# Performance work log

Measured on AMD Instinct MI355X. Metric: run time of the kernel, lower is better.

## Reference

```python
import jax, jax.numpy as jnp
import numpy as np

N_NODES = 100000
N_EDGES = 1600000
IN_C, HID_C, OUT_C = 128, 128, 64


def gcn_conv(x, W, b, src, dst, n_nodes):
    """PyG-style GCNConv: h = x @ W; add self-loops; symmetric deg^-1/2 norm;
    scatter-add aggregation; + bias. Self-loop contribution added analytically
    (norm for self-loop edge i->i is deg_i^-1) instead of materializing edges."""
    h = x @ W  # [N, C_out]
    # degree over dst including self-loops (edge weights are all ones)
    deg = jax.ops.segment_sum(jnp.ones((src.shape[0],), h.dtype), dst,
                              num_segments=n_nodes) + 1.0
    dinv = jax.lax.rsqrt(deg)  # deg >= 1 always
    norm = dinv[src] * dinv[dst]  # [E]
    agg = jax.ops.segment_sum(h[src] * norm[:, None], dst, num_segments=n_nodes)
    agg = agg + h * (dinv * dinv)[:, None]  # self-loop term
    return agg + b


def setup_inputs() -> dict:
    key = jax.random.key(0)
    k0, k1, k2, k3, k4, k5 = jax.random.split(key, 6)
    x = jax.random.normal(k0, (N_NODES, IN_C), dtype=jnp.float32)
    edge_index = jax.random.randint(k1, (2, N_EDGES), 0, N_NODES, dtype=jnp.int64)
    s1 = 1.0 / np.sqrt(IN_C)
    s2 = 1.0 / np.sqrt(HID_C)
    W1 = jax.random.uniform(k2, (IN_C, HID_C), jnp.float32, -s1, s1)
    b1 = jax.random.uniform(k3, (HID_C,), jnp.float32, -s1, s1)
    W2 = jax.random.uniform(k4, (HID_C, OUT_C), jnp.float32, -s2, s2)
    b2 = jax.random.uniform(k5, (OUT_C,), jnp.float32, -s2, s2)
    return {"x": x, "W1": W1, "b1": b1, "W2": W2, "b2": b2,
            "edge_index": edge_index}


def reference(x, W1, b1, W2, b2, edge_index):
    src, dst = edge_index[0], edge_index[1]
    h = gcn_conv(x, W1, b1, src, dst, N_NODES)
    h = jax.nn.relu(h)
    out = gcn_conv(h, W2, b2, src, dst, N_NODES)
    return out
```

## Files before the change

kernel.cpp:

```cpp
#include <hip/hip_runtime.h>


static constexpr int BSHIFT = 7;
static constexpr int BWIDTH = 1 << BSHIFT;
static constexpr int MAXBUCK = 2048;
static constexpr int NPART = 256;

static constexpr size_t OFF_ROW  = 458752;
static constexpr size_t OFF_CCNT = 925696;
static constexpr size_t OFF_COFF = 937984;
static constexpr size_t OFF_DINV = 962560;
static constexpr size_t OFF_CSR  = 1376256;
static constexpr size_t OFF_HS1  = 8388608;
static constexpr size_t OFF_OUT1 = 35651584;
static constexpr size_t OFF_HS2  = 62914560;
static constexpr size_t OFF_H2   = 75714560;
static constexpr size_t OFF_W1S  = 77811712;
static constexpr size_t OFF_W2S  = 77844480;

__device__ __forceinline__ unsigned short f2bf(float f) {
    unsigned u = __float_as_uint(f);
    u += 0x7fffu + ((u >> 16) & 1u);
    return (unsigned short)(u >> 16);
}

typedef __attribute__((ext_vector_type(8))) short bf16x8;
typedef __attribute__((ext_vector_type(4))) float f32x4;

__device__ __forceinline__ unsigned detect_flag(const unsigned* __restrict__ w) {
    unsigned fl = 0;
#pragma unroll
    for (int k = 1; k < 32; k += 2) fl |= w[k];
    return fl;
}

__device__ __forceinline__ int edge_dst(const unsigned* w, unsigned flag,
                                        int e, int E) {
    return flag ? (int)w[E + e] : (int)w[2 * E + 2 * e];
}
__device__ __forceinline__ int edge_src(const unsigned* w, unsigned flag,
                                        int e, int E) {
    return flag ? (int)w[e] : (int)w[2 * e];
}

__global__ __launch_bounds__(1024) void hist_wprep_kernel(
    const unsigned* __restrict__ w, unsigned* __restrict__ ccnt,
    unsigned* __restrict__ h2, int E, int nbuck,
    const float* __restrict__ W1, const float* __restrict__ W2,
    unsigned short* __restrict__ O1, unsigned short* __restrict__ O2) {
    if (blockIdx.x >= NPART) {
        const int which = blockIdx.x - NPART;
        const float* W = which ? W2 : W1;
        unsigned short* O = which ? O2 : O1;
        const int BN = which ? 64 : 128;
        const int total = 128 * BN / 4;
        for (int g = threadIdx.x; g < total; g += 1024) {
            int n = g % BN, k0 = (g / BN) * 4;
            ushort4 u;
            u.x = f2bf(W[(size_t)(k0 + 0) * BN + n]);
            u.y = f2bf(W[(size_t)(k0 + 1) * BN + n]);
            u.z = f2bf(W[(size_t)(k0 + 2) * BN + n]);
            u.w = f2bf(W[(size_t)(k0 + 3) * BN + n]);
            int off = ((((n >> 4) * 4 + (k0 >> 5)) * 16 + (n & 15)) * 4 +
                       ((k0 >> 3) & 3)) * 8 + (k0 & 4);
            *(ushort4*)(O + off) = u;
        }
        return;
    }
    __shared__ unsigned hist[MAXBUCK];
    for (int i = threadIdx.x; i < nbuck; i += 1024) hist[i] = 0;
    __syncthreads();
    const unsigned f = detect_flag(w);
    const int per = (E + NPART - 1) / NPART;
    const int e0 = blockIdx.x * per, e1 = min(E, e0 + per);
    for (int e = e0 + (int)threadIdx.x; e < e1; e += 1024)
        atomicAdd(&hist[edge_dst(w, f, e, E) >> BSHIFT], 1u);
    __syncthreads();
    for (int i = threadIdx.x; i < nbuck; i += 1024) {
        unsigned h = hist[i];
        h2[(size_t)i * NPART + blockIdx.x] = h;
        if (h) atomicAdd(&ccnt[i], h);
    }
}

__global__ __launch_bounds__(NPART) void scanoff_kernel(
    const unsigned* __restrict__ ccnt, unsigned* __restrict__ coff,
    unsigned* __restrict__ h2, int nbuck) {
    __shared__ unsigned red[NPART];
    __shared__ unsigned sh[NPART];
    const int b = blockIdx.x, t = threadIdx.x;
    unsigned p = 0;
    for (int i = t; i < b; i += NPART) p += ccnt[i];
    red[t] = p;
    __syncthreads();
#pragma unroll
    for (int off = NPART / 2; off > 0; off >>= 1) {
        if (t < off) red[t] += red[t + off];
        __syncthreads();
    }
    const unsigned coffb = red[0];
    if (t == 0) {
        coff[b] = coffb;
        if (b == nbuck - 1) coff[nbuck] = coffb + ccnt[b];
    }
    unsigned v = h2[(size_t)b * NPART + t];
    sh[t] = v;
    __syncthreads();
#pragma unroll
    for (int off = 1; off < NPART; off <<= 1) {
        unsigned a = (t >= off) ? sh[t - off] : 0u;
        __syncthreads();
        sh[t] += a;
        __syncthreads();
    }
    h2[(size_t)b * NPART + t] = coffb + sh[t] - v;
}

__global__ __launch_bounds__(1024) void partition_kernel(
    const unsigned* __restrict__ w, const unsigned* __restrict__ h2,
    unsigned* __restrict__ part, int E, int nbuck) {
    __shared__ unsigned lcur[MAXBUCK];
    for (int i = threadIdx.x; i < nbuck; i += 1024)
        lcur[i] = h2[(size_t)i * NPART + blockIdx.x];
    __syncthreads();
    const unsigned f = detect_flag(w);
    const int per = (E + NPART - 1) / NPART;
    const int e0 = blockIdx.x * per, e1 = min(E, e0 + per);
    for (int e = e0 + (int)threadIdx.x; e < e1; e += 1024) {
        int d = edge_dst(w, f, e, E);
        int s = edge_src(w, f, e, E);
        unsigned pos = atomicAdd(&lcur[d >> BSHIFT], 1u);
        part[pos] = (unsigned)s | ((unsigned)(d & (BWIDTH - 1)) << 20);
    }
}

template <int BN, bool ABF16, bool SCALE>
__device__ __forceinline__ void gemm_body(
    const void* __restrict__ Av, const unsigned short* __restrict__ Bs,
    const float* __restrict__ dinv, unsigned short* __restrict__ out,
    int M, int row0, int t) {
    constexpr int NT = BN / 16;
    const int w = t >> 6, lane = t & 63;
    const int m = lane & 15, q = lane >> 4;
    const int fb = (m * 4 + q) * 8;

    const int r0 = row0 + (2 * w) * 16 + m;
    const int r1 = r0 + 16;

    f32x4 acc[2][NT];
#pragma unroll
    for (int lt = 0; lt < 2; lt++)
#pragma unroll
        for (int nt = 0; nt < NT; nt++) acc[lt][nt] = (f32x4){0.f, 0.f, 0.f, 0.f};

#pragma unroll
    for (int ks = 0; ks < 4; ks++) {
        const int k0 = ks * 32 + q * 8;
        bf16x8 a0 = (bf16x8){0, 0, 0, 0, 0, 0, 0, 0};
        bf16x8 a1 = (bf16x8){0, 0, 0, 0, 0, 0, 0, 0};
        if (ABF16) {
            const unsigned short* A = (const unsigned short*)Av;
            if (r0 < M) a0 = *(const bf16x8*)(A + (size_t)r0 * 128 + k0);
            if (r1 < M) a1 = *(const bf16x8*)(A + (size_t)r1 * 128 + k0);
        } else {
            const float* A = (const float*)Av;
            if (r0 < M) {
                const float* p = A + (size_t)r0 * 128 + k0;
                f32x4 lo = *(const f32x4*)p, hi = *(const f32x4*)(p + 4);
                a0[0] = (short)f2bf(lo[0]); a0[1] = (short)f2bf(lo[1]);
                a0[2] = (short)f2bf(lo[2]); a0[3] = (short)f2bf(lo[3]);
                a0[4] = (short)f2bf(hi[0]); a0[5] = (short)f2bf(hi[1]);
                a0[6] = (short)f2bf(hi[2]); a0[7] = (short)f2bf(hi[3]);
            }
            if (r1 < M) {
                const float* p = A + (size_t)r1 * 128 + k0;
                f32x4 lo = *(const f32x4*)p, hi = *(const f32x4*)(p + 4);
                a1[0] = (short)f2bf(lo[0]); a1[1] = (short)f2bf(lo[1]);
                a1[2] = (short)f2bf(lo[2]); a1[3] = (short)f2bf(lo[3]);
                a1[4] = (short)f2bf(hi[0]); a1[5] = (short)f2bf(hi[1]);
                a1[6] = (short)f2bf(hi[2]); a1[7] = (short)f2bf(hi[3]);
            }
        }
#pragma unroll
        for (int nt = 0; nt < NT; nt++) {
            bf16x8 b = *(const bf16x8*)(Bs + (nt * 4 + ks) * 512 + fb);
            acc[0][nt] = __builtin_amdgcn_mfma_f32_16x16x32_bf16(a0, b, acc[0][nt], 0, 0, 0);
            acc[1][nt] = __builtin_amdgcn_mfma_f32_16x16x32_bf16(a1, b, acc[1][nt], 0, 0, 0);
        }
    }

#pragma unroll
    for (int lt = 0; lt < 2; lt++) {
#pragma unroll
        for (int r = 0; r < 4; r++) {
            int row = row0 + w * 32 + lt * 16 + q * 4 + r;
            if (row < M) {
                float s = SCALE ? dinv[row] : 1.0f;
#pragma unroll
                for (int nt = 0; nt < NT; nt++)
                    out[(size_t)row * BN + nt * 16 + m] = f2bf(acc[lt][nt][r] * s);
            }
        }
    }
}

template <int BN, bool ABF16>
__global__ __launch_bounds__(256) void gemm_mfma(
    const void* __restrict__ Av, const unsigned short* __restrict__ Bs,
    const float* __restrict__ dinv, unsigned short* __restrict__ out, int M) {
    gemm_body<BN, ABF16, true>(Av, Bs, dinv, out, M, blockIdx.x * 128,
                               threadIdx.x);
}

__global__ __launch_bounds__(256, 4) void bucket_gemm_kernel(
    const unsigned* __restrict__ part, const unsigned* __restrict__ coff,
    unsigned* __restrict__ row, float* __restrict__ dinv,
    int* __restrict__ csr, int N, int nbuck,
    const float* __restrict__ x, const unsigned short* __restrict__ w1s,
    unsigned short* __restrict__ hs1) {
    __shared__ unsigned cnt[BWIDTH];
    __shared__ unsigned sc[BWIDTH];
    __shared__ unsigned cur[BWIDTH];
    const int bid = blockIdx.x, t = threadIdx.x;
    if (bid >= nbuck) {
        gemm_body<128, false, false>(x, w1s, nullptr, hs1, N,
                                     (bid - nbuck) * 128, t);
        return;
    }
    const int b = bid, base = b << BSHIFT;
    if (t < BWIDTH) cnt[t] = 0;
    __syncthreads();
    const int e0 = (int)coff[b], e1 = (int)coff[b + 1];
    for (int e = e0 + t; e < e1; e += 256)
        atomicAdd(&cnt[part[e] >> 20], 1u);
    __syncthreads();
    if (t < BWIDTH) sc[t] = cnt[t];
    __syncthreads();
#pragma unroll
    for (int off = 1; off < BWIDTH; off <<= 1) {
        unsigned a = (t < BWIDTH && t >= off) ? sc[t - off] : 0u;
        __syncthreads();
        if (t < BWIDTH) sc[t] += a;
        __syncthreads();
    }
    if (t < BWIDTH) {
        unsigned r = (unsigned)e0 + sc[t] - cnt[t];
        cur[t] = r;
        if (base + t < N) {
            row[base + t] = r;
            dinv[base + t] = rsqrtf((float)cnt[t] + 1.0f);
        }
    }
    if (t == 0 && b == nbuck - 1) row[N] = (unsigned)e1;
    __syncthreads();
    for (int e = e0 + t; e < e1; e += 256) {
        unsigned pk = part[e];
        unsigned p = atomicAdd(&cur[pk >> 20], 1u);
        csr[p] = (int)(pk & 0xFFFFFu);
    }
}

template <int C, bool RELU, bool OUTBF, bool SCALED>
__global__ __launch_bounds__(256) void agg_kernel(
    const int* __restrict__ csr, const unsigned* __restrict__ row,
    const unsigned short* __restrict__ hsb, const float* __restrict__ dinv,
    const float* __restrict__ bias, void* __restrict__ outv, int N) {
    constexpr int LPN = C / 8;
    const int tid = blockIdx.x * 256 + threadIdx.x;
    const int i = tid / LPN;
    const int l = tid % LPN;
    if (i >= N) return;

    const int co = 8 * l;
    float s0 = 0.f, s1 = 0.f, s2 = 0.f, s3 = 0.f,
          s4 = 0.f, s5 = 0.f, s6 = 0.f, s7 = 0.f;
    {
        const float wsf = SCALED ? 1.f : dinv[i];
        uint4 u = *(const uint4*)(hsb + (size_t)i * C + co);
        s0 += wsf * __uint_as_float(u.x << 16);
        s1 += wsf * __uint_as_float(u.x & 0xffff0000u);
        s2 += wsf * __uint_as_float(u.y << 16);
        s3 += wsf * __uint_as_float(u.y & 0xffff0000u);
        s4 += wsf * __uint_as_float(u.z << 16);
        s5 += wsf * __uint_as_float(u.z & 0xffff0000u);
        s6 += wsf * __uint_as_float(u.w << 16);
        s7 += wsf * __uint_as_float(u.w & 0xffff0000u);
    }

    const int rs = (int)row[i], re = (int)row[i + 1];
    for (int e0 = rs; e0 < re; e0 += LPN) {
        int idx = (e0 + l < re) ? csr[e0 + l] : 0;
        const int cnt = min(LPN, re - e0);
#pragma unroll 4
        for (int j = 0; j < cnt; j++) {
            int s = __shfl(idx, j, LPN);
            const float wsr = SCALED ? 1.f : dinv[s];
            uint4 u = *(const uint4*)(hsb + (size_t)s * C + co);
            s0 += wsr * __uint_as_float(u.x << 16);
            s1 += wsr * __uint_as_float(u.x & 0xffff0000u);
            s2 += wsr * __uint_as_float(u.y << 16);
            s3 += wsr * __uint_as_float(u.y & 0xffff0000u);
            s4 += wsr * __uint_as_float(u.z << 16);
            s5 += wsr * __uint_as_float(u.z & 0xffff0000u);
            s6 += wsr * __uint_as_float(u.w << 16);
            s7 += wsr * __uint_as_float(u.w & 0xffff0000u);
        }
    }

    const float sc = dinv[i];
    const float4 ba = *(const float4*)(bias + co);
    const float4 bb = *(const float4*)(bias + co + 4);
    float o0 = s0 * sc + ba.x, o1 = s1 * sc + ba.y;
    float o2 = s2 * sc + ba.z, o3 = s3 * sc + ba.w;
    float o4 = s4 * sc + bb.x, o5 = s5 * sc + bb.y;
    float o6 = s6 * sc + bb.z, o7 = s7 * sc + bb.w;
    if (RELU) {
        o0 = fmaxf(o0, 0.f); o1 = fmaxf(o1, 0.f); o2 = fmaxf(o2, 0.f);
        o3 = fmaxf(o3, 0.f); o4 = fmaxf(o4, 0.f); o5 = fmaxf(o5, 0.f);
        o6 = fmaxf(o6, 0.f); o7 = fmaxf(o7, 0.f);
    }
    if (OUTBF) {
        uint4 u;
        u.x = (unsigned)f2bf(o0) | ((unsigned)f2bf(o1) << 16);
        u.y = (unsigned)f2bf(o2) | ((unsigned)f2bf(o3) << 16);
        u.z = (unsigned)f2bf(o4) | ((unsigned)f2bf(o5) << 16);
        u.w = (unsigned)f2bf(o6) | ((unsigned)f2bf(o7) << 16);
        *(uint4*)((unsigned short*)outv + (size_t)i * C + co) = u;
    } else {
        float4 a = make_float4(o0, o1, o2, o3);
        float4 b = make_float4(o4, o5, o6, o7);
        *(float4*)((float*)outv + (size_t)i * C + co) = a;
        *(float4*)((float*)outv + (size_t)i * C + co + 4) = b;
    }
}

extern "C" void kernel_launch(void* const* d_in, const int* in_sizes, int n_in,
                              void* d_out, int out_size, void* d_ws,
                              size_t ws_size, hipStream_t stream) {
    const float* x  = (const float*)d_in[0];
    const float* W1 = (const float*)d_in[1];
    const float* b1 = (const float*)d_in[2];
    const float* W2 = (const float*)d_in[3];
    const float* b2 = (const float*)d_in[4];
    const unsigned* ew = (const unsigned*)d_in[5];
    const int E = in_sizes[5] / 2;
    const int N = in_sizes[0] / 128;
    const int nbuck = (N + BWIDTH - 1) >> BSHIFT;

    char* ws = (char*)d_ws;
    unsigned* row  = (unsigned*)(ws + OFF_ROW);
    unsigned* ccnt = (unsigned*)(ws + OFF_CCNT);
    unsigned* coff = (unsigned*)(ws + OFF_COFF);
    float* dinv    = (float*)(ws + OFF_DINV);
    int* csr       = (int*)(ws + OFF_CSR);
    unsigned short* hs1  = (unsigned short*)(ws + OFF_HS1);
    unsigned short* out1 = (unsigned short*)(ws + OFF_OUT1);
    unsigned short* hs2  = (unsigned short*)(ws + OFF_HS2);
    unsigned* h2   = (unsigned*)(ws + OFF_H2);
    unsigned short* w1s  = (unsigned short*)(ws + OFF_W1S);
    unsigned short* w2s  = (unsigned short*)(ws + OFF_W2S);
    unsigned* part = (unsigned*)(ws + OFF_OUT1);

    hipMemsetAsync(ccnt, 0, (size_t)(nbuck + 1) * 4, stream);

    hist_wprep_kernel<<<NPART + 2, 1024, 0, stream>>>(ew, ccnt, h2, E, nbuck,
                                                      W1, W2, w1s, w2s);
    scanoff_kernel<<<nbuck, NPART, 0, stream>>>(ccnt, coff, h2, nbuck);
    partition_kernel<<<NPART, 1024, 0, stream>>>(ew, h2, part, E, nbuck);
    bucket_gemm_kernel<<<nbuck + (N + 127) / 128, 256, 0, stream>>>(
        part, coff, row, dinv, csr, N, nbuck, x, w1s, hs1);

    agg_kernel<128, true, true, false><<<(N * 16 + 255) / 256, 256, 0, stream>>>(
        csr, row, hs1, dinv, b1, out1, N);

    gemm_mfma<64, true><<<(N + 127) / 128, 256, 0, stream>>>(out1, w2s, dinv, hs2, N);
    agg_kernel<64, false, false, true><<<(N * 8 + 255) / 256, 256, 0, stream>>>(
        csr, row, hs2, dinv, b2, d_out, N);
}
```

Before: 274.4 us.

## Fuse layer-1 aggregation with layer-2 MFMA GEMM via shared-memory tile

Result: faster. 267.9 us (-2.4%).

```diff
diff --git a/kernel.cpp b/kernel.cpp
--- a/kernel.cpp
+++ b/kernel.cpp
@@ -12,7 +12,7 @@
 static constexpr size_t OFF_DINV = 962560;
 static constexpr size_t OFF_CSR  = 1376256;
 static constexpr size_t OFF_HS1  = 8388608;
-static constexpr size_t OFF_OUT1 = 35651584;
+static constexpr size_t OFF_PART = 35651584;
 static constexpr size_t OFF_HS2  = 62914560;
 static constexpr size_t OFF_H2   = 75714560;
 static constexpr size_t OFF_W1S  = 77811712;
@@ -204,14 +204,6 @@
     }
 }
 
-template <int BN, bool ABF16>
-__global__ __launch_bounds__(256) void gemm_mfma(
-    const void* __restrict__ Av, const unsigned short* __restrict__ Bs,
-    const float* __restrict__ dinv, unsigned short* __restrict__ out, int M) {
-    gemm_body<BN, ABF16, true>(Av, Bs, dinv, out, M, blockIdx.x * 128,
-                               threadIdx.x);
-}
-
 __global__ __launch_bounds__(256, 4) void bucket_gemm_kernel(
     const unsigned* __restrict__ part, const unsigned* __restrict__ coff,
     unsigned* __restrict__ row, float* __restrict__ dinv,
@@ -260,12 +252,99 @@
     }
 }
 
-template <int C, bool RELU, bool OUTBF, bool SCALED>
-__global__ __launch_bounds__(256) void agg_kernel(
+__global__ __launch_bounds__(256) void agg_gemm_kernel(
+    const int* __restrict__ csr, const unsigned* __restrict__ row,
+    const unsigned short* __restrict__ hs1, const float* __restrict__ dinv,
+    const float* __restrict__ bias, const unsigned short* __restrict__ w2s,
+    unsigned short* __restrict__ hs2, int N) {
+    __shared__ short sA[2048];
+    const int t = threadIdx.x;
+    const int i0 = blockIdx.x * 16;
+    const int i = i0 + (t >> 4);
+    const int l = t & 15;
+
+    float s0 = 0.f, s1 = 0.f, s2 = 0.f, s3 = 0.f,
+          s4 = 0.f, s5 = 0.f, s6 = 0.f, s7 = 0.f;
+    if (i < N) {
+        const int co = 8 * l;
+        {
+            const float wsf = dinv[i];
+            uint4 u = *(const uint4*)(hs1 + (size_t)i * 128 + co);
+            s0 += wsf * __uint_as_float(u.x << 16);
+            s1 += wsf * __uint_as_float(u.x & 0xffff0000u);
+            s2 += wsf * __uint_as_float(u.y << 16);
+            s3 += wsf * __uint_as_float(u.y & 0xffff0000u);
+            s4 += wsf * __uint_as_float(u.z << 16);
+            s5 += wsf * __uint_as_float(u.z & 0xffff0000u);
+            s6 += wsf * __uint_as_float(u.w << 16);
+            s7 += wsf * __uint_as_float(u.w & 0xffff0000u);
+        }
+        const int rs = (int)row[i], re = (int)row[i + 1];
+        for (int e0 = rs; e0 < re; e0 += 16) {
+            int idx = (e0 + l < re) ? csr[e0 + l] : 0;
+            const int cnt = min(16, re - e0);
+#pragma unroll 4
+            for (int j = 0; j < cnt; j++) {
+                int s = __shfl(idx, j, 16);
+                const float wsr = dinv[s];
+                uint4 u = *(const uint4*)(hs1 + (size_t)s * 128 + co);
+                s0 += wsr * __uint_as_float(u.x << 16);
+                s1 += wsr * __uint_as_float(u.x & 0xffff0000u);
+                s2 += wsr * __uint_as_float(u.y << 16);
+                s3 += wsr * __uint_as_float(u.y & 0xffff0000u);
+                s4 += wsr * __uint_as_float(u.z << 16);
+                s5 += wsr * __uint_as_float(u.z & 0xffff0000u);
+                s6 += wsr * __uint_as_float(u.w << 16);
+                s7 += wsr * __uint_as_float(u.w & 0xffff0000u);
+            }
+        }
+        const float sc = dinv[i];
+        const int co2 = 8 * l;
+        const float4 ba = *(const float4*)(bias + co2);
+        const float4 bb = *(const float4*)(bias + co2 + 4);
+        s0 = fmaxf(s0 * sc + ba.x, 0.f); s1 = fmaxf(s1 * sc + ba.y, 0.f);
+        s2 = fmaxf(s2 * sc + ba.z, 0.f); s3 = fmaxf(s3 * sc + ba.w, 0.f);
+        s4 = fmaxf(s4 * sc + bb.x, 0.f); s5 = fmaxf(s5 * sc + bb.y, 0.f);
+        s6 = fmaxf(s6 * sc + bb.z, 0.f); s7 = fmaxf(s7 * sc + bb.w, 0.f);
+    } else {
+        s0 = s1 = s2 = s3 = s4 = s5 = s6 = s7 = 0.f;
+    }
+    {
+        uint4 u;
+        u.x = (unsigned)f2bf(s0) | ((unsigned)f2bf(s1) << 16);
+        u.y = (unsigned)f2bf(s2) | ((unsigned)f2bf(s3) << 16);
+        u.z = (unsigned)f2bf(s4) | ((unsigned)f2bf(s5) << 16);
+        u.w = (unsigned)f2bf(s6) | ((unsigned)f2bf(s7) << 16);
+        int off = (l >> 2) * 512 + (((t >> 4) * 4 + (l & 3)) * 8);
+        *(uint4*)(sA + off) = u;
+    }
+    __syncthreads();
+
+    const int w = t >> 6, lane = t & 63;
+    const int m = lane & 15, q = lane >> 4;
+    const int fb = (m * 4 + q) * 8;
+    f32x4 acc = (f32x4){0.f, 0.f, 0.f, 0.f};
+#pragma unroll
+    for (int ks = 0; ks < 4; ks++) {
+        bf16x8 a = *(const bf16x8*)(sA + ks * 512 + fb);
+        bf16x8 b = *(const bf16x8*)(w2s + (w * 4 + ks) * 512 + fb);
+        acc = __builtin_amdgcn_mfma_f32_16x16x32_bf16(a, b, acc, 0, 0, 0);
+    }
+#pragma unroll
+    for (int r = 0; r < 4; r++) {
+        int rr = i0 + q * 4 + r;
+        if (rr < N) {
+            float s = dinv[rr];
+            hs2[(size_t)rr * 64 + w * 16 + m] = f2bf(acc[r] * s);
+        }
+    }
+}
+
+__global__ __launch_bounds__(256) void agg2_kernel(
     const int* __restrict__ csr, const unsigned* __restrict__ row,
     const unsigned short* __restrict__ hsb, const float* __restrict__ dinv,
-    const float* __restrict__ bias, void* __restrict__ outv, int N) {
-    constexpr int LPN = C / 8;
+    const float* __restrict__ bias, float* __restrict__ outv, int N) {
+    constexpr int C = 64, LPN = 8;
     const int tid = blockIdx.x * 256 + threadIdx.x;
     const int i = tid / LPN;
     const int l = tid % LPN;
@@ -275,16 +354,11 @@
     float s0 = 0.f, s1 = 0.f, s2 = 0.f, s3 = 0.f,
           s4 = 0.f, s5 = 0.f, s6 = 0.f, s7 = 0.f;
     {
-        const float wsf = SCALED ? 1.f : dinv[i];
         uint4 u = *(const uint4*)(hsb + (size_t)i * C + co);
-        s0 += wsf * __uint_as_float(u.x << 16);
-        s1 += wsf * __uint_as_float(u.x & 0xffff0000u);
-        s2 += wsf * __uint_as_float(u.y << 16);
-        s3 += wsf * __uint_as_float(u.y & 0xffff0000u);
-        s4 += wsf * __uint_as_float(u.z << 16);
-        s5 += wsf * __uint_as_float(u.z & 0xffff0000u);
-        s6 += wsf * __uint_as_float(u.w << 16);
-        s7 += wsf * __uint_as_float(u.w & 0xffff0000u);
+        s0 += __uint_as_float(u.x << 16); s1 += __uint_as_float(u.x & 0xffff0000u);
+        s2 += __uint_as_float(u.y << 16); s3 += __uint_as_float(u.y & 0xffff0000u);
+        s4 += __uint_as_float(u.z << 16); s5 += __uint_as_float(u.z & 0xffff0000u);
+        s6 += __uint_as_float(u.w << 16); s7 += __uint_as_float(u.w & 0xffff0000u);
     }
 
     const int rs = (int)row[i], re = (int)row[i + 1];
@@ -294,44 +368,23 @@
 #pragma unroll 4
         for (int j = 0; j < cnt; j++) {
             int s = __shfl(idx, j, LPN);
-            const float wsr = SCALED ? 1.f : dinv[s];
             uint4 u = *(const uint4*)(hsb + (size_t)s * C + co);
-            s0 += wsr * __uint_as_float(u.x << 16);
-            s1 += wsr * __uint_as_float(u.x & 0xffff0000u);
-            s2 += wsr * __uint_as_float(u.y << 16);
-            s3 += wsr * __uint_as_float(u.y & 0xffff0000u);
-            s4 += wsr * __uint_as_float(u.z << 16);
-            s5 += wsr * __uint_as_float(u.z & 0xffff0000u);
-            s6 += wsr * __uint_as_float(u.w << 16);
-            s7 += wsr * __uint_as_float(u.w & 0xffff0000u);
+            s0 += __uint_as_float(u.x << 16); s1 += __uint_as_float(u.x & 0xffff0000u);
+            s2 += __uint_as_float(u.y << 16); s3 += __uint_as_float(u.y & 0xffff0000u);
+            s4 += __uint_as_float(u.z << 16); s5 += __uint_as_float(u.z & 0xffff0000u);
+            s6 += __uint_as_float(u.w << 16); s7 += __uint_as_float(u.w & 0xffff0000u);
         }
     }
 
     const float sc = dinv[i];
     const float4 ba = *(const float4*)(bias + co);
     const float4 bb = *(const float4*)(bias + co + 4);
-    float o0 = s0 * sc + ba.x, o1 = s1 * sc + ba.y;
-    float o2 = s2 * sc + ba.z, o3 = s3 * sc + ba.w;
-    float o4 = s4 * sc + bb.x, o5 = s5 * sc + bb.y;
-    float o6 = s6 * sc + bb.z, o7 = s7 * sc + bb.w;
-    if (RELU) {
-        o0 = fmaxf(o0, 0.f); o1 = fmaxf(o1, 0.f); o2 = fmaxf(o2, 0.f);
-        o3 = fmaxf(o3, 0.f); o4 = fmaxf(o4, 0.f); o5 = fmaxf(o5, 0.f);
-        o6 = fmaxf(o6, 0.f); o7 = fmaxf(o7, 0.f);
-    }
-    if (OUTBF) {
-        uint4 u;
-        u.x = (unsigned)f2bf(o0) | ((unsigned)f2bf(o1) << 16);
-        u.y = (unsigned)f2bf(o2) | ((unsigned)f2bf(o3) << 16);
-        u.z = (unsigned)f2bf(o4) | ((unsigned)f2bf(o5) << 16);
-        u.w = (unsigned)f2bf(o6) | ((unsigned)f2bf(o7) << 16);
-        *(uint4*)((unsigned short*)outv + (size_t)i * C + co) = u;
-    } else {
-        float4 a = make_float4(o0, o1, o2, o3);
-        float4 b = make_float4(o4, o5, o6, o7);
-        *(float4*)((float*)outv + (size_t)i * C + co) = a;
-        *(float4*)((float*)outv + (size_t)i * C + co + 4) = b;
-    }
+    float4 a = make_float4(s0 * sc + ba.x, s1 * sc + ba.y,
+                           s2 * sc + ba.z, s3 * sc + ba.w);
+    float4 b = make_float4(s4 * sc + bb.x, s5 * sc + bb.y,
+                           s6 * sc + bb.z, s7 * sc + bb.w);
+    *(float4*)(outv + (size_t)i * C + co) = a;
+    *(float4*)(outv + (size_t)i * C + co + 4) = b;
 }
 
 extern "C" void kernel_launch(void* const* d_in, const int* in_sizes, int n_in,
@@ -354,12 +407,11 @@
     float* dinv    = (float*)(ws + OFF_DINV);
     int* csr       = (int*)(ws + OFF_CSR);
     unsigned short* hs1  = (unsigned short*)(ws + OFF_HS1);
-    unsigned short* out1 = (unsigned short*)(ws + OFF_OUT1);
     unsigned short* hs2  = (unsigned short*)(ws + OFF_HS2);
     unsigned* h2   = (unsigned*)(ws + OFF_H2);
     unsigned short* w1s  = (unsigned short*)(ws + OFF_W1S);
     unsigned short* w2s  = (unsigned short*)(ws + OFF_W2S);
-    unsigned* part = (unsigned*)(ws + OFF_OUT1);
+    unsigned* part = (unsigned*)(ws + OFF_PART);
 
     hipMemsetAsync(ccnt, 0, (size_t)(nbuck + 1) * 4, stream);
 
@@ -370,10 +422,9 @@
     bucket_gemm_kernel<<<nbuck + (N + 127) / 128, 256, 0, stream>>>(
         part, coff, row, dinv, csr, N, nbuck, x, w1s, hs1);
 
-    agg_kernel<128, true, true, false><<<(N * 16 + 255) / 256, 256, 0, stream>>>(
-        csr, row, hs1, dinv, b1, out1, N);
-
-    gemm_mfma<64, true><<<(N + 127) / 128, 256, 0, stream>>>(out1, w2s, dinv, hs2, N);
-    agg_kernel<64, false, false, true><<<(N * 8 + 255) / 256, 256, 0, stream>>>(
-        csr, row, hs2, dinv, b2, d_out, N);
-}
+    agg_gemm_kernel<<<(N + 15) / 16, 256, 0, stream>>>(
+        csr, row, hs1, dinv, b1, w2s, hs2, N);
+
+    agg2_kernel<<<(N * 8 + 255) / 256, 256, 0, stream>>>(
+        csr, row, hs2, dinv, b2, (float*)d_out, N);
+}
```
